# Optimization experiments

Hardware: AMD Instinct MI355X
Metric: run time of the kernel (lower is better)

Reference implementation:

```python
import jax, jax.numpy as jnp
import numpy as np

B, N, H, HS = 8, 96, 8, 32
NS = H * HS  # 256, also ES
EPS = 1e-5


def _linear(x, w, b):
    return x @ w + b  # w: [in, out]


def _ln(x, g, b):
    m = jnp.mean(x, axis=-1, keepdims=True)
    v = jnp.var(x, axis=-1, keepdims=True)
    return (x - m) * jax.lax.rsqrt(v + EPS) * g + b


def _sep_n(x):  # [B,N,NS] -> [B,H,N,HS]
    b, n, _ = x.shape
    return x.reshape(b, n, H, HS).transpose(0, 2, 1, 3)


def _sep_e(x):  # [B,N,N,ES] -> [B,H,N,N,HS]
    b, n, _, _ = x.shape
    return x.reshape(b, n, n, H, HS).transpose(0, 3, 1, 2, 4)


def setup_inputs() -> dict:
    key = jax.random.key(0)
    ks = jax.random.split(key, 32)
    s = 1.0 / np.sqrt(NS)
    d = {
        "node_tensors": jax.random.normal(ks[0], (B, N, NS), jnp.float32),
        "edge_tensors": jax.random.normal(ks[1], (B, N, N, NS), jnp.float32),
    }
    names = ["Wn", "We", "Wn1", "Wn2", "Wee"]
    for i, nm in enumerate(names):
        d[nm + "_w"] = jax.random.uniform(ks[2 + 2 * i], (3, NS, NS), jnp.float32, -s, s)
        d[nm + "_b"] = jax.random.uniform(ks[3 + 2 * i], (3, NS), jnp.float32, -s, s)
    for i, nm in enumerate(["NL1", "NL2", "EL1", "EL2"]):
        d[nm + "_w"] = jax.random.uniform(ks[12 + 2 * i], (NS, NS), jnp.float32, -s, s)
        d[nm + "_b"] = jax.random.uniform(ks[13 + 2 * i], (NS,), jnp.float32, -s, s)
    d["NLN1_g"] = jnp.ones((NS,), jnp.float32)
    d["NLN1_b"] = jnp.zeros((NS,), jnp.float32)
    d["ELN1_g"] = jnp.ones((NS,), jnp.float32)
    d["ELN1_b"] = jnp.zeros((NS,), jnp.float32)
    return d


def _forward(node_tensors, edge_tensors, Wn_w, Wn_b, We_w, We_b, Wn1_w, Wn1_b,
             Wn2_w, Wn2_b, Wee_w, Wee_b, NL1_w, NL1_b, NL2_w, NL2_b,
             EL1_w, EL1_b, EL2_w, EL2_b, NLN1_g, NLN1_b, ELN1_g, ELN1_b):
    scale = 1.0 / jnp.sqrt(jnp.float32(HS))
    b = node_tensors.shape[0]

    # --- node attention ---
    eQ = _sep_e(_linear(edge_tensors, We_w[0], We_b[0]))
    eK = _sep_e(_linear(edge_tensors, We_w[1], We_b[1]))
    eV = _sep_e(_linear(edge_tensors, We_w[2], We_b[2]))
    nQ = _sep_n(_linear(node_tensors, Wn_w[0], Wn_b[0]))
    nK = _sep_n(_linear(node_tensors, Wn_w[1], Wn_b[1]))
    nV = _sep_n(_linear(node_tensors, Wn_w[2], Wn_b[2]))

    Q = eQ + nQ[:, :, :, None, :]          # [B,H,N,N,HS]
    K = eK + nK[:, :, None, :, :]
    scores = jnp.einsum('bhijc,bhijc->bhij', Q, K) * scale
    attn = jax.nn.softmax(scores, axis=-1)
    V = eV + nV[:, :, None, :, :]
    new_nodes = jnp.einsum('bhij,bhijc->bhic', attn, V)   # [B,H,N,HS]
    attw = new_nodes.transpose(0, 2, 1, 3).reshape(b, N, NS)

    res = _linear(jax.nn.relu(_linear(attw, NL1_w, NL1_b)), NL2_w, NL2_b)
    node_out = _ln(node_tensors + res, NLN1_g, NLN1_b)

    # --- edge update ---
    n1Q = _sep_n(_linear(node_out, Wn1_w[0], Wn1_b[0]))
    n1K = _sep_n(_linear(node_out, Wn1_w[1], Wn1_b[1]))
    n1V = _sep_n(_linear(node_out, Wn1_w[2], Wn1_b[2]))
    n2Q = _sep_n(_linear(node_out, Wn2_w[0], Wn2_b[0]))
    n2K = _sep_n(_linear(node_out, Wn2_w[1], Wn2_b[1]))
    n2V = _sep_n(_linear(node_out, Wn2_w[2], Wn2_b[2]))
    eQe = _sep_e(_linear(edge_tensors, Wee_w[0], Wee_b[0]))
    eKe = _sep_e(_linear(edge_tensors, Wee_w[1], Wee_b[1]))
    eVe = _sep_e(_linear(edge_tensors, Wee_w[2], Wee_b[2]))

    Qe = eQe + n1Q[:, :, :, None, :] + n2Q[:, :, None, :, :]
    Ke = eKe + n1K[:, :, :, None, :] + n2K[:, :, None, :, :]
    se = jnp.einsum('bhijc,bhijc->bhij', Qe, Ke) * scale
    attn_e = jax.nn.silu(se)                               # [B,H,N,N]
    Ve = eVe + n1V[:, :, :, None, :] + n2V[:, :, None, :, :]
    new_edges = attn_e[..., None] * Ve                     # [B,H,N,N,HS]
    attw_e = new_edges.transpose(0, 2, 3, 1, 4).reshape(b, N, N, NS)

    res_e = _linear(jax.nn.relu(_linear(attw_e, EL1_w, EL1_b)), EL2_w, EL2_b)
    edge_out = _ln(edge_tensors + res_e, ELN1_g, ELN1_b)
    return node_out, edge_out


def reference(node_tensors, edge_tensors, Wn_w, Wn_b, We_w, We_b, Wn1_w, Wn1_b,
              Wn2_w, Wn2_b, Wee_w, Wee_b, NL1_w, NL1_b, NL2_w, NL2_b,
              EL1_w, EL1_b, EL2_w, EL2_b, NLN1_g, NLN1_b, ELN1_g, ELN1_b):
    return _forward(node_tensors, edge_tensors, Wn_w, Wn_b, We_w, We_b,
                    Wn1_w, Wn1_b, Wn2_w, Wn2_b, Wee_w, Wee_b, NL1_w, NL1_b,
                    NL2_w, NL2_b, EL1_w, EL1_b, EL2_w, EL2_b,
                    NLN1_g, NLN1_b, ELN1_g, ELN1_b)
```

## Files before the change

### kernel.cpp

```cpp
#include <hip/hip_runtime.h>


#define DI __device__ __forceinline__

typedef float f32x4 __attribute__((ext_vector_type(4)));
typedef short bf16x8 __attribute__((ext_vector_type(8)));

DI unsigned short f2bf(float f) {
  union { float f; unsigned u; } v; v.f = f;
  return (unsigned short)((v.u + 0x7FFFu + ((v.u >> 16) & 1u)) >> 16);
}
DI float bf2f(unsigned short h) {
  union { unsigned u; float f; } v; v.u = ((unsigned)h) << 16;
  return v.f;
}

#define LDE 264
#define SCALE 0.17677669529663687f

#define MFMA(A, B, C) __builtin_amdgcn_mfma_f32_16x16x32_bf16((A), (B), (C), 0, 0, 0)

__global__ __launch_bounds__(256)
void prep_and_qkv(const float* __restrict__ We_w, const float* __restrict__ Wee_w,
                  const float* __restrict__ EL1_w, const float* __restrict__ EL2_w,
                  const float* __restrict__ NL1_w, const float* __restrict__ NL2_w,
                  const float* __restrict__ Wn1_w, const float* __restrict__ Wn2_w,
                  unsigned short* __restrict__ fb,
                  const float* __restrict__ node, const float* __restrict__ Ww,
                  const float* __restrict__ Wb, float* __restrict__ nQ,
                  float* __restrict__ nK, float* __restrict__ nV)
{
  __shared__ float Wl[32 * 256];
  const int t = threadIdx.x;
  if (blockIdx.x < 128) {
    const int blk = blockIdx.x, kt = blk & 7, ms = blk >> 3;
    const float* src; unsigned short* dst; int NT, ntbase;
    if (ms < 3)       { src = We_w  + ms * 65536;        dst = fb;          NT = 48; ntbase = ms * 16; }
    else if (ms < 6)  { src = Wee_w + (ms - 3) * 65536;  dst = fb + 196608; NT = 48; ntbase = (ms - 3) * 16; }
    else if (ms == 6) { src = EL1_w;                     dst = fb + 393216; NT = 16; ntbase = 0; }
    else if (ms == 7) { src = EL2_w;                     dst = fb + 458752; NT = 16; ntbase = 0; }
    else if (ms == 8) { src = NL1_w;                     dst = fb + 524288; NT = 16; ntbase = 0; }
    else if (ms == 9) { src = NL2_w;                     dst = fb + 589824; NT = 16; ntbase = 0; }
    else if (ms < 13) { src = Wn1_w + (ms - 10) * 65536; dst = fb + 655360; NT = 48; ntbase = (ms - 10) * 16; }
    else              { src = Wn2_w + (ms - 13) * 65536; dst = fb + 851968; NT = 48; ntbase = (ms - 13) * 16; }
    for (int u = t; u < 32 * 64; u += 256) {
      const int r = u >> 6, c4 = (u & 63) << 2;
      *(float4*)(Wl + r * 256 + c4) = *(const float4*)(src + (kt * 32 + r) * 256 + c4);
    }
    __syncthreads();
    for (int u = t; u < 16 * 64; u += 256) {
      const int ntl = u >> 6, l = u & 63;
      const int kb = (l >> 4) << 3, c = ntl * 16 + (l & 15);
      unsigned short tmp[8];
      #pragma unroll
      for (int i = 0; i < 8; ++i) tmp[i] = f2bf(Wl[(kb + i) * 256 + c]);
      const int nt = ntbase + ntl;
      *(uint4*)(dst + ((size_t)(kt * NT + nt) * 64 + l) * 8) = *(const uint4*)tmp;
    }
  } else {
    float (*x)[256] = (float(*)[256])Wl;
    const int r0 = (blockIdx.x - 128) * 4;
    #pragma unroll
    for (int rr = 0; rr < 4; ++rr) x[rr][t] = node[(r0 + rr) * 256 + t];
    __syncthreads();
    float a0[4], a1[4], a2[4];
    #pragma unroll
    for (int rr = 0; rr < 4; ++rr) { a0[rr] = Wb[t]; a1[rr] = Wb[256 + t]; a2[rr] = Wb[512 + t]; }
    for (int k = 0; k < 256; ++k) {
      const float w0 = Ww[k * 256 + t], w1 = Ww[65536 + k * 256 + t], w2 = Ww[131072 + k * 256 + t];
      #pragma unroll
      for (int rr = 0; rr < 4; ++rr) {
        const float xv = x[rr][k];
        a0[rr] += xv * w0; a1[rr] += xv * w1; a2[rr] += xv * w2;
      }
    }
    const int h = t >> 5, c = t & 31;
    #pragma unroll
    for (int rr = 0; rr < 4; ++rr) {
      const int row = r0 + rr, b = row / 96, j = row - b * 96;
      const int oi = ((b * 8 + h) * 96 + j) * 32 + c;
      nQ[oi] = a0[rr]; nK[oi] = a1[rr]; nV[oi] = a2[rr];
    }
  }
}

__global__ __launch_bounds__(512, 2)
void node_attn(const float* __restrict__ edge, const float* __restrict__ We_b,
               const unsigned short* __restrict__ WeF,
               const float* __restrict__ nQ, const float* __restrict__ nK,
               const float* __restrict__ nV, float* __restrict__ attw)
{
  __shared__ unsigned short Elds[96 * LDE];
  __shared__ float sc[768];
  __shared__ float nQp[256];
  __shared__ float bias[768];

  const int tid = threadIdx.x, lane = tid & 63, wid = tid >> 6;
  const int b = blockIdx.x & 7, i = blockIdx.x >> 3;
  const size_t bi = (size_t)(b * 96 + i);

  if (tid < 256) nQp[tid] = nQ[((b * 8 + (tid >> 5)) * 96 + i) * 32 + (tid & 31)];
  for (int u = tid; u < 768; u += 512) bias[u] = We_b[u];

  const float* Erow = edge + bi * 24576;
  for (int u = tid; u < 96 * 64; u += 512) {
    const int j = u >> 6, g = u & 63;
    const float4 v = *(const float4*)(Erow + j * 256 + g * 4);
    const unsigned lo = (unsigned)f2bf(v.x) | ((unsigned)f2bf(v.y) << 16);
    const unsigned hi = (unsigned)f2bf(v.z) | ((unsigned)f2bf(v.w) << 16);
    *(uint2*)(Elds + j * LDE + g * 4) = make_uint2(lo, hi);
  }
  __syncthreads();

  {
    const int h = wid;
    const unsigned short* wq0 = WeF + ((2 * h) * 64 + lane) * 8;
    const unsigned short* wq1 = WeF + ((2 * h + 1) * 64 + lane) * 8;
    const unsigned short* wk0 = WeF + ((16 + 2 * h) * 64 + lane) * 8;
    const unsigned short* wk1 = WeF + ((17 + 2 * h) * 64 + lane) * 8;
    const int c0 = h * 32 + (lane & 15), c1 = c0 + 16;
    const float qb0 = bias[c0] + nQp[c0], qb1 = bias[c1] + nQp[c1];
    const float kb0 = bias[256 + c0], kb1 = bias[256 + c1];
    for (int pass = 0; pass < 2; ++pass) {
      const f32x4 z = {0.f, 0.f, 0.f, 0.f};
      f32x4 aq0[3] = {z, z, z}, aq1[3] = {z, z, z}, ak0[3] = {z, z, z}, ak1[3] = {z, z, z};
      __builtin_amdgcn_s_setprio(1);
      for (int kt = 0; kt < 8; ++kt) {
        const bf16x8 b0 = *(const bf16x8*)(wq0 + kt * 24576);
        const bf16x8 b1 = *(const bf16x8*)(wq1 + kt * 24576);
        const bf16x8 b2 = *(const bf16x8*)(wk0 + kt * 24576);
        const bf16x8 b3 = *(const bf16x8*)(wk1 + kt * 24576);
        #pragma unroll
        for (int m = 0; m < 3; ++m) {
          const int mt = pass * 3 + m;
          const bf16x8 afr = *(const bf16x8*)(Elds + (mt * 16 + (lane & 15)) * LDE
                                              + ((lane >> 4) << 3) + kt * 32);
          aq0[m] = MFMA(afr, b0, aq0[m]);
          aq1[m] = MFMA(afr, b1, aq1[m]);
          ak0[m] = MFMA(afr, b2, ak0[m]);
          ak1[m] = MFMA(afr, b3, ak1[m]);
        }
      }
      __builtin_amdgcn_s_setprio(0);
      #pragma unroll
      for (int m = 0; m < 3; ++m) {
        const int mt = pass * 3 + m;
        float prod[4];
        #pragma unroll
        for (int r = 0; r < 4; ++r) {
          const int j = mt * 16 + ((lane >> 4) << 2) + r;
          const int g = ((b * 8 + h) * 96 + j) * 32;
          const float k0v = ak0[m][r] + kb0 + nK[g + (lane & 15)];
          const float k1v = ak1[m][r] + kb1 + nK[g + 16 + (lane & 15)];
          prod[r] = (aq0[m][r] + qb0) * k0v + (aq1[m][r] + qb1) * k1v;
        }
        #pragma unroll
        for (int mm = 1; mm < 16; mm <<= 1) {
          #pragma unroll
          for (int r = 0; r < 4; ++r) prod[r] += __shfl_xor(prod[r], mm, 64);
        }
        if ((lane & 15) == 0) {
          #pragma unroll
          for (int r = 0; r < 4; ++r)
            sc[h * 96 + mt * 16 + ((lane >> 4) << 2) + r] = prod[r];
        }
      }
    }
  }

  const f32x4 z = {0.f, 0.f, 0.f, 0.f};
  f32x4 accB[6][2] = {{z, z}, {z, z}, {z, z}, {z, z}, {z, z}, {z, z}};
  {
    const unsigned short* wb0 = WeF + ((32 + wid) * 64 + lane) * 8;
    const unsigned short* wb1 = WeF + ((40 + wid) * 64 + lane) * 8;
    __builtin_amdgcn_s_setprio(1);
    for (int kt = 0; kt < 8; ++kt) {
      const bf16x8 b0 = *(const bf16x8*)(wb0 + kt * 24576);
      const bf16x8 b1 = *(const bf16x8*)(wb1 + kt * 24576);
      #pragma unroll
      for (int mt = 0; mt < 6; ++mt) {
        const bf16x8 afr = *(const bf16x8*)(Elds + (mt * 16 + (lane & 15)) * LDE
                                            + ((lane >> 4) << 3) + kt * 32);
        accB[mt][0] = MFMA(afr, b0, accB[mt][0]);
        accB[mt][1] = MFMA(afr, b1, accB[mt][1]);
      }
    }
    __builtin_amdgcn_s_setprio(0);
  }
  __syncthreads();

  {
    const int h = wid;
    const float s0 = sc[h * 96 + lane] * SCALE;
    const float s1 = (lane < 32) ? sc[h * 96 + 64 + lane] * SCALE : -1e30f;
    float mx = fmaxf(s0, s1);
    #pragma unroll
    for (int m = 1; m < 64; m <<= 1) mx = fmaxf(mx, __shfl_xor(mx, m, 64));
    const float e0 = __expf(s0 - mx);
    const float e1 = (lane < 32) ? __expf(s1 - mx) : 0.f;
    float sm = e0 + e1;
    #pragma unroll
    for (int m = 1; m < 64; m <<= 1) sm += __shfl_xor(sm, m, 64);
    const float inv = 1.f / sm;
    sc[h * 96 + lane] = e0 * inv;
    if (lane < 32) sc[h * 96 + 64 + lane] = e1 * inv;
  }
  __syncthreads();

  {
    const int col0 = wid * 16 + (lane & 15), col1 = col0 + 128;
    const int h0 = col0 >> 5, cc0 = col0 & 31;
    const int h1 = col1 >> 5, cc1 = col1 & 31;
    const float base0 = bias[512 + col0], base1 = bias[512 + col1];
    float nn[2] = {0.f, 0.f};
    #pragma unroll
    for (int mt = 0; mt < 6; ++mt) {
      #pragma unroll
      for (int r = 0; r < 4; ++r) {
        const int j = mt * 16 + ((lane >> 4) << 2) + r;
        const float v0 = accB[mt][0][r] + base0 + nV[((b * 8 + h0) * 96 + j) * 32 + cc0];
        const float v1 = accB[mt][1][r] + base1 + nV[((b * 8 + h1) * 96 + j) * 32 + cc1];
        nn[0] += sc[h0 * 96 + j] * v0;
        nn[1] += sc[h1 * 96 + j] * v1;
      }
    }
    #pragma unroll
    for (int s = 0; s < 2; ++s) {
      nn[s] += __shfl_xor(nn[s], 16, 64);
      nn[s] += __shfl_xor(nn[s], 32, 64);
    }
    if (lane < 16) {
      attw[bi * 256 + wid * 16 + lane] = nn[0];
      attw[bi * 256 + (wid + 8) * 16 + lane] = nn[1];
    }
  }
}

__global__ __launch_bounds__(256)
void node_tail(const float* __restrict__ attw, const float* __restrict__ node,
               const unsigned short* __restrict__ NL1F, const float* __restrict__ B1,
               const unsigned short* __restrict__ NL2F, const float* __restrict__ B2,
               const float* __restrict__ g, const float* __restrict__ be,
               const unsigned short* __restrict__ Wn1F, const float* __restrict__ P1b,
               const unsigned short* __restrict__ Wn2F, const float* __restrict__ P2b,
               float* __restrict__ node_out,
               float* __restrict__ n1Q, float* __restrict__ n1K, float* __restrict__ n1V,
               float* __restrict__ n2Q, float* __restrict__ n2K, float* __restrict__ n2V)
{
  __shared__ unsigned short Xl[16 * LDE];
  __shared__ unsigned short Hl[16 * LDE];
  __shared__ float bb[1024];
  __shared__ float p1b[768], p2b[768];
  __shared__ float psum[4][16], psq[4][16];
  __shared__ float statm[16], statr[16];

  const int t = threadIdx.x, lane = t & 63, w = t >> 6;
  const int bt = blockIdx.x, r0 = bt * 16;
  const int b = bt / 6, nbase = (bt % 6) * 16;

  bb[t] = B1[t]; bb[256 + t] = B2[t]; bb[512 + t] = g[t]; bb[768 + t] = be[t];
  for (int u = t; u < 768; u += 256) { p1b[u] = P1b[u]; p2b[u] = P2b[u]; }

  for (int u = t; u < 16 * 64; u += 256) {
    const int j = u >> 6, gg = u & 63;
    const float4 v = *(const float4*)(attw + (size_t)(r0 + j) * 256 + gg * 4);
    const unsigned lo = (unsigned)f2bf(v.x) | ((unsigned)f2bf(v.y) << 16);
    const unsigned hi = (unsigned)f2bf(v.z) | ((unsigned)f2bf(v.w) << 16);
    *(uint2*)(Xl + j * LDE + gg * 4) = make_uint2(lo, hi);
  }
  __syncthreads();

  const f32x4 z = {0.f, 0.f, 0.f, 0.f};

  {
    f32x4 a1[4] = {z, z, z, z};
    for (int kt = 0; kt < 8; ++kt) {
      const bf16x8 afr = *(const bf16x8*)(Xl + (lane & 15) * LDE + ((lane >> 4) << 3) + kt * 32);
      #pragma unroll
      for (int p = 0; p < 4; ++p) {
        const bf16x8 bf = *(const bf16x8*)(NL1F + (((kt << 4) + (w * 4 + p)) * 64 + lane) * 8);
        a1[p] = MFMA(afr, bf, a1[p]);
      }
    }
    #pragma unroll
    for (int p = 0; p < 4; ++p) {
      const int col = (w * 4 + p) * 16 + (lane & 15);
      const float bv = bb[col];
      #pragma unroll
      for (int r = 0; r < 4; ++r) {
        const int j = ((lane >> 4) << 2) + r;
        Hl[j * LDE + col] = f2bf(fmaxf(a1[p][r] + bv, 0.f));
      }
    }
  }
  __syncthreads();

  float xv[4][4];
  {
    f32x4 a2[4] = {z, z, z, z};
    for (int kt = 0; kt < 8; ++kt) {
      const bf16x8 afr = *(const bf16x8*)(Hl + (lane & 15) * LDE + ((lane >> 4) << 3) + kt * 32);
      #pragma unroll
      for (int p = 0; p < 4; ++p) {
        const bf16x8 bf = *(const bf16x8*)(NL2F + (((kt << 4) + (w * 4 + p)) * 64 + lane) * 8);
        a2[p] = MFMA(afr, bf, a2[p]);
      }
    }
    #pragma unroll
    for (int p = 0; p < 4; ++p) {
      const int col = (w * 4 + p) * 16 + (lane & 15);
      const float bv = bb[256 + col];
      #pragma unroll
      for (int r = 0; r < 4; ++r) {
        const int j = ((lane >> 4) << 2) + r;
        xv[p][r] = a2[p][r] + bv + node[(size_t)(r0 + j) * 256 + col];
      }
    }
    #pragma unroll
    for (int r = 0; r < 4; ++r) {
      float s = 0.f, q = 0.f;
      #pragma unroll
      for (int p = 0; p < 4; ++p) { s += xv[p][r]; q += xv[p][r] * xv[p][r]; }
      #pragma unroll
      for (int m = 1; m < 16; m <<= 1) { s += __shfl_xor(s, m, 64); q += __shfl_xor(q, m, 64); }
      if ((lane & 15) == 0) {
        const int rl = ((lane >> 4) << 2) + r;
        psum[w][rl] = s; psq[w][rl] = q;
      }
    }
  }
  __syncthreads();
  if (t < 16) {
    const float s = psum[0][t] + psum[1][t] + psum[2][t] + psum[3][t];
    const float q = psq[0][t] + psq[1][t] + psq[2][t] + psq[3][t];
    const float mean = s * (1.f / 256.f);
    statm[t] = mean;
    statr[t] = rsqrtf(q * (1.f / 256.f) - mean * mean + 1e-5f);
  }
  __syncthreads();
  #pragma unroll
  for (int p = 0; p < 4; ++p) {
    const int col = (w * 4 + p) * 16 + (lane & 15);
    const float gv = bb[512 + col], bv = bb[768 + col];
    #pragma unroll
    for (int r = 0; r < 4; ++r) {
      const int j = ((lane >> 4) << 2) + r;
      const float o = (xv[p][r] - statm[j]) * statr[j] * gv + bv;
      node_out[(size_t)(r0 + j) * 256 + col] = o;
      Xl[j * LDE + col] = f2bf(o);
    }
  }
  __syncthreads();

  bf16x8 xfr[8];
  #pragma unroll
  for (int kt = 0; kt < 8; ++kt)
    xfr[kt] = *(const bf16x8*)(Xl + (lane & 15) * LDE + ((lane >> 4) << 3) + kt * 32);
  #pragma unroll
  for (int ps = 0; ps < 2; ++ps) {
    const unsigned short* WF = ps ? Wn2F : Wn1F;
    const float* pb = ps ? p2b : p1b;
    f32x4 ac[12] = {z, z, z, z, z, z, z, z, z, z, z, z};
    __builtin_amdgcn_s_setprio(1);
    for (int kt = 0; kt < 8; ++kt) {
      #pragma unroll
      for (int m = 0; m < 12; ++m) {
        const int nt = w * 12 + m;
        const bf16x8 bf = *(const bf16x8*)(WF + ((kt * 48 + nt) * 64 + lane) * 8);
        ac[m] = MFMA(xfr[kt], bf, ac[m]);
      }
    }
    __builtin_amdgcn_s_setprio(0);
    #pragma unroll
    for (int m = 0; m < 12; ++m) {
      const int nt = w * 12 + m;
      const int colg = nt * 16 + (lane & 15);
      const int q = colg >> 8, cn = colg & 255, h = cn >> 5, c = cn & 31;
      float* o = (q == 0) ? (ps ? n2Q : n1Q)
               : (q == 1) ? (ps ? n2K : n1K)
                          : (ps ? n2V : n1V);
      const float bv = pb[colg];
      #pragma unroll
      for (int r = 0; r < 4; ++r) {
        const int j = ((lane >> 4) << 2) + r;
        o[((b * 8 + h) * 96 + nbase + j) * 32 + c] = ac[m][r] + bv;
      }
    }
  }
}

__global__ __launch_bounds__(512, 2)
void edge_update(const float* __restrict__ edge, const float* __restrict__ Wee_b,
                 const unsigned short* __restrict__ WeeF,
                 const unsigned short* __restrict__ EL1F,
                 const unsigned short* __restrict__ EL2F,
                 const float* __restrict__ EL1_b, const float* __restrict__ EL2_b,
                 const float* __restrict__ n1Q, const float* __restrict__ n1K, const float* __restrict__ n1V,
                 const float* __restrict__ n2Q, const float* __restrict__ n2K, const float* __restrict__ n2V,
                 const float* __restrict__ lng, const float* __restrict__ lnb,
                 float* __restrict__ edge_out)
{
  __shared__ unsigned short Elds[96 * LDE];
  __shared__ float se[768];
  __shared__ float bn1[768];
  __shared__ float b12[512];
  __shared__ float lg[256], lb[256];

  const int tid = threadIdx.x, lane = tid & 63, wid = tid >> 6;
  const int b = blockIdx.x & 7, i = blockIdx.x >> 3;
  const size_t bi = (size_t)(b * 96 + i);

  for (int u = tid; u < 768; u += 512) {
    const int q = u >> 8, cn = u & 255, h = cn >> 5, c = cn & 31;
    const float* s = (q == 0) ? n1Q : (q == 1) ? n1K : n1V;
    bn1[u] = Wee_b[u] + s[((b * 8 + h) * 96 + i) * 32 + c];
  }
  b12[tid] = (tid < 256) ? EL1_b[tid] : EL2_b[tid - 256];
  if (tid < 256) { lg[tid] = lng[tid]; lb[tid] = lnb[tid]; }

  const float* Erow = edge + bi * 24576;
  for (int u = tid; u < 96 * 64; u += 512) {
    const int j = u >> 6, g = u & 63;
    const float4 v = *(const float4*)(Erow + j * 256 + g * 4);
    const unsigned lo = (unsigned)f2bf(v.x) | ((unsigned)f2bf(v.y) << 16);
    const unsigned hi = (unsigned)f2bf(v.z) | ((unsigned)f2bf(v.w) << 16);
    *(uint2*)(Elds + j * LDE + g * 4) = make_uint2(lo, hi);
  }
  __syncthreads();

  {
    const int h = wid;
    const unsigned short* wq0 = WeeF + ((2 * h) * 64 + lane) * 8;
    const unsigned short* wq1 = WeeF + ((2 * h + 1) * 64 + lane) * 8;
    const unsigned short* wk0 = WeeF + ((16 + 2 * h) * 64 + lane) * 8;
    const unsigned short* wk1 = WeeF + ((17 + 2 * h) * 64 + lane) * 8;
    const int c0 = h * 32 + (lane & 15), c1 = c0 + 16;
    const float qb0 = bn1[c0], qb1 = bn1[c1];
    const float kb0 = bn1[256 + c0], kb1 = bn1[256 + c1];
    for (int pass = 0; pass < 2; ++pass) {
      const f32x4 z = {0.f, 0.f, 0.f, 0.f};
      f32x4 aq0[3] = {z, z, z}, aq1[3] = {z, z, z}, ak0[3] = {z, z, z}, ak1[3] = {z, z, z};
      __builtin_amdgcn_s_setprio(1);
      for (int kt = 0; kt < 8; ++kt) {
        const bf16x8 b0 = *(const bf16x8*)(wq0 + kt * 24576);
        const bf16x8 b1 = *(const bf16x8*)(wq1 + kt * 24576);
        const bf16x8 b2 = *(const bf16x8*)(wk0 + kt * 24576);
        const bf16x8 b3 = *(const bf16x8*)(wk1 + kt * 24576);
        #pragma unroll
        for (int m = 0; m < 3; ++m) {
          const int mt = pass * 3 + m;
          const bf16x8 afr = *(const bf16x8*)(Elds + (mt * 16 + (lane & 15)) * LDE
                                              + ((lane >> 4) << 3) + kt * 32);
          aq0[m] = MFMA(afr, b0, aq0[m]);
          aq1[m] = MFMA(afr, b1, aq1[m]);
          ak0[m] = MFMA(afr, b2, ak0[m]);
          ak1[m] = MFMA(afr, b3, ak1[m]);
        }
      }
      __builtin_amdgcn_s_setprio(0);
      #pragma unroll
      for (int m = 0; m < 3; ++m) {
        const int mt = pass * 3 + m;
        float prod[4];
        #pragma unroll
        for (int r = 0; r < 4; ++r) {
          const int j = mt * 16 + ((lane >> 4) << 2) + r;
          const int g = ((b * 8 + h) * 96 + j) * 32;
          const float q0v = aq0[m][r] + qb0 + n2Q[g + (lane & 15)];
          const float q1v = aq1[m][r] + qb1 + n2Q[g + 16 + (lane & 15)];
          const float k0v = ak0[m][r] + kb0 + n2K[g + (lane & 15)];
          const float k1v = ak1[m][r] + kb1 + n2K[g + 16 + (lane & 15)];
          prod[r] = q0v * k0v + q1v * k1v;
        }
        #pragma unroll
        for (int mm = 1; mm < 16; mm <<= 1) {
          #pragma unroll
          for (int r = 0; r < 4; ++r) prod[r] += __shfl_xor(prod[r], mm, 64);
        }
        if ((lane & 15) == 0) {
          #pragma unroll
          for (int r = 0; r < 4; ++r) {
            const float d = prod[r] * SCALE;
            se[h * 96 + mt * 16 + ((lane >> 4) << 2) + r] = d / (1.f + __expf(-d));
          }
        }
      }
    }
  }

  const f32x4 z = {0.f, 0.f, 0.f, 0.f};
  f32x4 acc[6][2] = {{z, z}, {z, z}, {z, z}, {z, z}, {z, z}, {z, z}};
  {
    const unsigned short* wb0 = WeeF + ((32 + wid) * 64 + lane) * 8;
    const unsigned short* wb1 = WeeF + ((40 + wid) * 64 + lane) * 8;
    __builtin_amdgcn_s_setprio(1);
    for (int kt = 0; kt < 8; ++kt) {
      const bf16x8 b0 = *(const bf16x8*)(wb0 + kt * 24576);
      const bf16x8 b1 = *(const bf16x8*)(wb1 + kt * 24576);
      #pragma unroll
      for (int mt = 0; mt < 6; ++mt) {
        const bf16x8 afr = *(const bf16x8*)(Elds + (mt * 16 + (lane & 15)) * LDE
                                            + ((lane >> 4) << 3) + kt * 32);
        acc[mt][0] = MFMA(afr, b0, acc[mt][0]);
        acc[mt][1] = MFMA(afr, b1, acc[mt][1]);
      }
    }
    __builtin_amdgcn_s_setprio(0);
  }
  __syncthreads();

  {
    const int col0 = wid * 16 + (lane & 15), col1 = col0 + 128;
    const int h0 = col0 >> 5, cc0 = col0 & 31;
    const int h1 = col1 >> 5, cc1 = col1 & 31;
    const float base0 = bn1[512 + col0], base1 = bn1[512 + col1];
    #pragma unroll
    for (int mt = 0; mt < 6; ++mt) {
      #pragma unroll
      for (int r = 0; r < 4; ++r) {
        const int j = mt * 16 + ((lane >> 4) << 2) + r;
        const float v0 = acc[mt][0][r] + base0 + n2V[((b * 8 + h0) * 96 + j) * 32 + cc0];
        const float v1 = acc[mt][1][r] + base1 + n2V[((b * 8 + h1) * 96 + j) * 32 + cc1];
        Elds[j * LDE + col0] = f2bf(se[h0 * 96 + j] * v0);
        Elds[j * LDE + col1] = f2bf(se[h1 * 96 + j] * v1);
      }
    }
  }
  __syncthreads();

  {
    #pragma unroll
    for (int mt = 0; mt < 6; ++mt) { acc[mt][0] = z; acc[mt][1] = z; }
    const unsigned short* wb0 = EL1F + (wid * 64 + lane) * 8;
    const unsigned short* wb1 = EL1F + ((wid + 8) * 64 + lane) * 8;
    __builtin_amdgcn_s_setprio(1);
    for (int kt = 0; kt < 8; ++kt) {
      const bf16x8 b0 = *(const bf16x8*)(wb0 + kt * 8192);
      const bf16x8 b1 = *(const bf16x8*)(wb1 + kt * 8192);
      #pragma unroll
      for (int mt = 0; mt < 6; ++mt) {
        const bf16x8 afr = *(const bf16x8*)(Elds + (mt * 16 + (lane & 15)) * LDE
                                            + ((lane >> 4) << 3) + kt * 32);
        acc[mt][0] = MFMA(afr, b0, acc[mt][0]);
        acc[mt][1] = MFMA(afr, b1, acc[mt][1]);
      }
    }
    __builtin_amdgcn_s_setprio(0);
    __syncthreads();
    const int col0 = wid * 16 + (lane & 15), col1 = col0 + 128;
    const float bv0 = b12[col0], bv1 = b12[col1];
    #pragma unroll
    for (int mt = 0; mt < 6; ++mt) {
      #pragma unroll
      for (int r = 0; r < 4; ++r) {
        const int j = mt * 16 + ((lane >> 4) << 2) + r;
        Elds[j * LDE + col0] = f2bf(fmaxf(acc[mt][0][r] + bv0, 0.f));
        Elds[j * LDE + col1] = f2bf(fmaxf(acc[mt][1][r] + bv1, 0.f));
      }
    }
  }
  __syncthreads();

  {
    #pragma unroll
    for (int mt = 0; mt < 6; ++mt) { acc[mt][0] = z; acc[mt][1] = z; }
    const unsigned short* wb0 = EL2F + (wid * 64 + lane) * 8;
    const unsigned short* wb1 = EL2F + ((wid + 8) * 64 + lane) * 8;
    __builtin_amdgcn_s_setprio(1);
    for (int kt = 0; kt < 8; ++kt) {
      const bf16x8 b0 = *(const bf16x8*)(wb0 + kt * 8192);
      const bf16x8 b1 = *(const bf16x8*)(wb1 + kt * 8192);
      #pragma unroll
      for (int mt = 0; mt < 6; ++mt) {
        const bf16x8 afr = *(const bf16x8*)(Elds + (mt * 16 + (lane & 15)) * LDE
                                            + ((lane >> 4) << 3) + kt * 32);
        acc[mt][0] = MFMA(afr, b0, acc[mt][0]);
        acc[mt][1] = MFMA(afr, b1, acc[mt][1]);
      }
    }
    __builtin_amdgcn_s_setprio(0);
    const int col0 = wid * 16 + (lane & 15), col1 = col0 + 128;
    const float bv0 = b12[256 + col0], bv1 = b12[256 + col1];
    const float g0 = lg[col0], g1 = lg[col1], be0 = lb[col0], be1 = lb[col1];
    __syncthreads();
    #pragma unroll
    for (int mt = 0; mt < 6; ++mt) {
      #pragma unroll
      for (int r = 0; r < 4; ++r) {
        const int j = mt * 16 + ((lane >> 4) << 2) + r;
        acc[mt][0][r] += bv0 + Erow[j * 256 + col0];
        acc[mt][1][r] += bv1 + Erow[j * 256 + col1];
      }
    }
    #pragma unroll
    for (int mt = 0; mt < 6; ++mt) {
      #pragma unroll
      for (int r = 0; r < 4; ++r) {
        float s = acc[mt][0][r] + acc[mt][1][r];
        float q = acc[mt][0][r] * acc[mt][0][r] + acc[mt][1][r] * acc[mt][1][r];
        #pragma unroll
        for (int m = 1; m < 16; m <<= 1) { s += __shfl_xor(s, m, 64); q += __shfl_xor(q, m, 64); }
        if ((lane & 15) == 0) {
          const int j = mt * 16 + ((lane >> 4) << 2) + r;
          se[wid * 96 + j] = s; bn1[wid * 96 + j] = q;
        }
      }
    }
    __syncthreads();
    if (tid < 96) {
      float s = 0.f, q = 0.f;
      #pragma unroll
      for (int w = 0; w < 8; ++w) { s += se[w * 96 + tid]; q += bn1[w * 96 + tid]; }
      const float mean = s * (1.f / 256.f);
      b12[tid] = mean;
      b12[96 + tid] = rsqrtf(q * (1.f / 256.f) - mean * mean + 1e-5f);
    }
    __syncthreads();
    #pragma unroll
    for (int mt = 0; mt < 6; ++mt) {
      #pragma unroll
      for (int r = 0; r < 4; ++r) {
        const int j = mt * 16 + ((lane >> 4) << 2) + r;
        const float mean = b12[j], rs = b12[96 + j];
        Elds[j * LDE + col0] = f2bf((acc[mt][0][r] - mean) * rs * g0 + be0);
        Elds[j * LDE + col1] = f2bf((acc[mt][1][r] - mean) * rs * g1 + be1);
      }
    }
  }
  __syncthreads();

  float* orow = edge_out + bi * 24576;
  for (int j = wid; j < 96; j += 8) {
    const uint2 pk = *(const uint2*)(Elds + j * LDE + (lane << 2));
    float4 o;
    o.x = bf2f((unsigned short)(pk.x & 0xffff));
    o.y = bf2f((unsigned short)(pk.x >> 16));
    o.z = bf2f((unsigned short)(pk.y & 0xffff));
    o.w = bf2f((unsigned short)(pk.y >> 16));
    *(float4*)(orow + j * 256 + (lane << 2)) = o;
  }
}

extern "C" void kernel_launch(void* const* d_in, const int* in_sizes, int n_in,
                              void* d_out, int out_size, void* d_ws, size_t ws_size,
                              hipStream_t stream)
{
  (void)in_sizes; (void)n_in; (void)out_size; (void)ws_size;

  const float* node   = (const float*)d_in[0];
  const float* edge   = (const float*)d_in[1];
  const float* Wn_w   = (const float*)d_in[2];
  const float* Wn_b   = (const float*)d_in[3];
  const float* We_w   = (const float*)d_in[4];
  const float* We_b   = (const float*)d_in[5];
  const float* Wn1_w  = (const float*)d_in[6];
  const float* Wn1_b  = (const float*)d_in[7];
  const float* Wn2_w  = (const float*)d_in[8];
  const float* Wn2_b  = (const float*)d_in[9];
  const float* Wee_w  = (const float*)d_in[10];
  const float* Wee_b  = (const float*)d_in[11];
  const float* NL1_w  = (const float*)d_in[12];
  const float* NL1_b  = (const float*)d_in[13];
  const float* NL2_w  = (const float*)d_in[14];
  const float* NL2_b  = (const float*)d_in[15];
  const float* EL1_w  = (const float*)d_in[16];
  const float* EL1_b  = (const float*)d_in[17];
  const float* EL2_w  = (const float*)d_in[18];
  const float* EL2_b  = (const float*)d_in[19];
  const float* NLN1_g = (const float*)d_in[20];
  const float* NLN1_b = (const float*)d_in[21];
  const float* ELN1_g = (const float*)d_in[22];
  const float* ELN1_b = (const float*)d_in[23];

  float* out = (float*)d_out;
  float* node_out = out;
  float* edge_out = out + 196608;

  float* wsf = (float*)d_ws;
  float* nQ  = wsf;                float* nK  = wsf + 196608;   float* nV  = wsf + 393216;
  float* n1Q = wsf + 589824;       float* n1K = wsf + 786432;   float* n1V = wsf + 983040;
  float* n2Q = wsf + 1179648;      float* n2K = wsf + 1376256;  float* n2V = wsf + 1572864;
  float* attw = wsf + 1769472;
  unsigned short* fb   = (unsigned short*)(wsf + 1966080);
  unsigned short* WeF  = fb;
  unsigned short* WeeF = fb + 196608;
  unsigned short* EL1F = fb + 393216;
  unsigned short* EL2F = fb + 458752;
  unsigned short* NL1F = fb + 524288;
  unsigned short* NL2F = fb + 589824;
  unsigned short* Wn1F = fb + 655360;
  unsigned short* Wn2F = fb + 851968;

  prep_and_qkv<<<320, 256, 0, stream>>>(We_w, Wee_w, EL1_w, EL2_w,
                                        NL1_w, NL2_w, Wn1_w, Wn2_w, fb,
                                        node, Wn_w, Wn_b, nQ, nK, nV);
  node_attn<<<768, 512, 0, stream>>>(edge, We_b, WeF, nQ, nK, nV, attw);
  node_tail<<<48, 256, 0, stream>>>(attw, node, NL1F, NL1_b, NL2F, NL2_b,
                                    NLN1_g, NLN1_b, Wn1F, Wn1_b, Wn2F, Wn2_b,
                                    node_out, n1Q, n1K, n1V, n2Q, n2K, n2V);
  edge_update<<<768, 512, 0, stream>>>(edge, Wee_b, WeeF, EL1F, EL2F,
                                       EL1_b, EL2_b, n1Q, n1K, n1V,
                                       n2Q, n2K, n2V, ELN1_g, ELN1_b, edge_out);
}
```

Measured before the change: 261.4 us.

## Split node QKV into MFMA kernel, shrink edge_update LDS for higher occupancy

```diff
diff --git a/kernel.cpp b/kernel.cpp
--- a/kernel.cpp
+++ b/kernel.cpp
@@ -21,65 +21,87 @@
 #define MFMA(A, B, C) __builtin_amdgcn_mfma_f32_16x16x32_bf16((A), (B), (C), 0, 0, 0)
 
 __global__ __launch_bounds__(256)
-void prep_and_qkv(const float* __restrict__ We_w, const float* __restrict__ Wee_w,
-                  const float* __restrict__ EL1_w, const float* __restrict__ EL2_w,
-                  const float* __restrict__ NL1_w, const float* __restrict__ NL2_w,
-                  const float* __restrict__ Wn1_w, const float* __restrict__ Wn2_w,
-                  unsigned short* __restrict__ fb,
-                  const float* __restrict__ node, const float* __restrict__ Ww,
-                  const float* __restrict__ Wb, float* __restrict__ nQ,
-                  float* __restrict__ nK, float* __restrict__ nV)
+void prep_frags(const float* __restrict__ We_w, const float* __restrict__ Wee_w,
+                const float* __restrict__ EL1_w, const float* __restrict__ EL2_w,
+                const float* __restrict__ NL1_w, const float* __restrict__ NL2_w,
+                const float* __restrict__ Wn1_w, const float* __restrict__ Wn2_w,
+                const float* __restrict__ Wn_w,
+                unsigned short* __restrict__ fb)
 {
   __shared__ float Wl[32 * 256];
   const int t = threadIdx.x;
-  if (blockIdx.x < 128) {
-    const int blk = blockIdx.x, kt = blk & 7, ms = blk >> 3;
-    const float* src; unsigned short* dst; int NT, ntbase;
-    if (ms < 3)       { src = We_w  + ms * 65536;        dst = fb;          NT = 48; ntbase = ms * 16; }
-    else if (ms < 6)  { src = Wee_w + (ms - 3) * 65536;  dst = fb + 196608; NT = 48; ntbase = (ms - 3) * 16; }
-    else if (ms == 6) { src = EL1_w;                     dst = fb + 393216; NT = 16; ntbase = 0; }
-    else if (ms == 7) { src = EL2_w;                     dst = fb + 458752; NT = 16; ntbase = 0; }
-    else if (ms == 8) { src = NL1_w;                     dst = fb + 524288; NT = 16; ntbase = 0; }
-    else if (ms == 9) { src = NL2_w;                     dst = fb + 589824; NT = 16; ntbase = 0; }
-    else if (ms < 13) { src = Wn1_w + (ms - 10) * 65536; dst = fb + 655360; NT = 48; ntbase = (ms - 10) * 16; }
-    else              { src = Wn2_w + (ms - 13) * 65536; dst = fb + 851968; NT = 48; ntbase = (ms - 13) * 16; }
-    for (int u = t; u < 32 * 64; u += 256) {
-      const int r = u >> 6, c4 = (u & 63) << 2;
-      *(float4*)(Wl + r * 256 + c4) = *(const float4*)(src + (kt * 32 + r) * 256 + c4);
-    }
-    __syncthreads();
-    for (int u = t; u < 16 * 64; u += 256) {
-      const int ntl = u >> 6, l = u & 63;
-      const int kb = (l >> 4) << 3, c = ntl * 16 + (l & 15);
-      unsigned short tmp[8];
-      #pragma unroll
-      for (int i = 0; i < 8; ++i) tmp[i] = f2bf(Wl[(kb + i) * 256 + c]);
-      const int nt = ntbase + ntl;
-      *(uint4*)(dst + ((size_t)(kt * NT + nt) * 64 + l) * 8) = *(const uint4*)tmp;
-    }
-  } else {
-    float (*x)[256] = (float(*)[256])Wl;
-    const int r0 = (blockIdx.x - 128) * 4;
-    #pragma unroll
-    for (int rr = 0; rr < 4; ++rr) x[rr][t] = node[(r0 + rr) * 256 + t];
-    __syncthreads();
-    float a0[4], a1[4], a2[4];
-    #pragma unroll
-    for (int rr = 0; rr < 4; ++rr) { a0[rr] = Wb[t]; a1[rr] = Wb[256 + t]; a2[rr] = Wb[512 + t]; }
-    for (int k = 0; k < 256; ++k) {
-      const float w0 = Ww[k * 256 + t], w1 = Ww[65536 + k * 256 + t], w2 = Ww[131072 + k * 256 + t];
-      #pragma unroll
-      for (int rr = 0; rr < 4; ++rr) {
-        const float xv = x[rr][k];
-        a0[rr] += xv * w0; a1[rr] += xv * w1; a2[rr] += xv * w2;
-      }
-    }
-    const int h = t >> 5, c = t & 31;
-    #pragma unroll
-    for (int rr = 0; rr < 4; ++rr) {
-      const int row = r0 + rr, b = row / 96, j = row - b * 96;
-      const int oi = ((b * 8 + h) * 96 + j) * 32 + c;
-      nQ[oi] = a0[rr]; nK[oi] = a1[rr]; nV[oi] = a2[rr];
+  const int blk = blockIdx.x, kt = blk & 7, ms = blk >> 3;
+  const float* src; unsigned short* dst; int NT, ntbase;
+  if (ms < 3)       { src = We_w  + ms * 65536;        dst = fb;           NT = 48; ntbase = ms * 16; }
+  else if (ms < 6)  { src = Wee_w + (ms - 3) * 65536;  dst = fb + 196608;  NT = 48; ntbase = (ms - 3) * 16; }
+  else if (ms == 6) { src = EL1_w;                     dst = fb + 393216;  NT = 16; ntbase = 0; }
+  else if (ms == 7) { src = EL2_w;                     dst = fb + 458752;  NT = 16; ntbase = 0; }
+  else if (ms == 8) { src = NL1_w;                     dst = fb + 524288;  NT = 16; ntbase = 0; }
+  else if (ms == 9) { src = NL2_w;                     dst = fb + 589824;  NT = 16; ntbase = 0; }
+  else if (ms < 13) { src = Wn1_w + (ms - 10) * 65536; dst = fb + 655360;  NT = 48; ntbase = (ms - 10) * 16; }
+  else if (ms < 16) { src = Wn2_w + (ms - 13) * 65536; dst = fb + 851968;  NT = 48; ntbase = (ms - 13) * 16; }
+  else              { src = Wn_w  + (ms - 16) * 65536; dst = fb + 1048576; NT = 48; ntbase = (ms - 16) * 16; }
+  for (int u = t; u < 32 * 64; u += 256) {
+    const int r = u >> 6, c4 = (u & 63) << 2;
+    *(float4*)(Wl + r * 256 + c4) = *(const float4*)(src + (kt * 32 + r) * 256 + c4);
+  }
+  __syncthreads();
+  for (int u = t; u < 16 * 64; u += 256) {
+    const int ntl = u >> 6, l = u & 63;
+    const int kb = (l >> 4) << 3, c = ntl * 16 + (l & 15);
+    unsigned short tmp[8];
+    #pragma unroll
+    for (int i = 0; i < 8; ++i) tmp[i] = f2bf(Wl[(kb + i) * 256 + c]);
+    const int nt = ntbase + ntl;
+    *(uint4*)(dst + ((size_t)(kt * NT + nt) * 64 + l) * 8) = *(const uint4*)tmp;
+  }
+}
+
+__global__ __launch_bounds__(256)
+void node_qkv(const float* __restrict__ node, const unsigned short* __restrict__ WnF,
+              const float* __restrict__ Wb, float* __restrict__ nQ,
+              float* __restrict__ nK, float* __restrict__ nV)
+{
+  __shared__ unsigned short Xl[16 * LDE];
+  const int t = threadIdx.x, lane = t & 63, w = t >> 6;
+  const int rb = blockIdx.x, r0 = rb * 16;
+  const int b = rb / 6, nbase = (rb % 6) * 16;
+
+  for (int u = t; u < 16 * 64; u += 256) {
+    const int j = u >> 6, gg = u & 63;
+    const float4 v = *(const float4*)(node + (size_t)(r0 + j) * 256 + gg * 4);
+    const unsigned lo = (unsigned)f2bf(v.x) | ((unsigned)f2bf(v.y) << 16);
+    const unsigned hi = (unsigned)f2bf(v.z) | ((unsigned)f2bf(v.w) << 16);
+    *(uint2*)(Xl + j * LDE + gg * 4) = make_uint2(lo, hi);
+  }
+  __syncthreads();
+
+  const f32x4 z = {0.f, 0.f, 0.f, 0.f};
+  bf16x8 xfr[8];
+  #pragma unroll
+  for (int kt = 0; kt < 8; ++kt)
+    xfr[kt] = *(const bf16x8*)(Xl + (lane & 15) * LDE + ((lane >> 4) << 3) + kt * 32);
+  f32x4 ac[12] = {z, z, z, z, z, z, z, z, z, z, z, z};
+  __builtin_amdgcn_s_setprio(1);
+  for (int kt = 0; kt < 8; ++kt) {
+    #pragma unroll
+    for (int m = 0; m < 12; ++m) {
+      const int nt = w * 12 + m;
+      const bf16x8 bf = *(const bf16x8*)(WnF + ((kt * 48 + nt) * 64 + lane) * 8);
+      ac[m] = MFMA(xfr[kt], bf, ac[m]);
+    }
+  }
+  __builtin_amdgcn_s_setprio(0);
+  #pragma unroll
+  for (int m = 0; m < 12; ++m) {
+    const int colg = (w * 12 + m) * 16 + (lane & 15);
+    const int q = colg >> 8, cn = colg & 255, h = cn >> 5, c = cn & 31;
+    float* o = (q == 0) ? nQ : (q == 1) ? nK : nV;
+    const float bv = Wb[colg];
+    #pragma unroll
+    for (int r = 0; r < 4; ++r) {
+      const int j = ((lane >> 4) << 2) + r;
+      o[((b * 8 + h) * 96 + nbase + j) * 32 + c] = ac[m][r] + bv;
     }
   }
 }
@@ -250,16 +272,14 @@
   __shared__ unsigned short Xl[16 * LDE];
   __shared__ unsigned short Hl[16 * LDE];
   __shared__ float bb[1024];
-  __shared__ float p1b[768], p2b[768];
   __shared__ float psum[4][16], psq[4][16];
   __shared__ float statm[16], statr[16];
 
   const int t = threadIdx.x, lane = t & 63, w = t >> 6;
-  const int bt = blockIdx.x, r0 = bt * 16;
-  const int b = bt / 6, nbase = (bt % 6) * 16;
+  const int ps = blockIdx.x & 1, rb = blockIdx.x >> 1;
+  const int r0 = rb * 16, b = rb / 6, nbase = (rb % 6) * 16;
 
   bb[t] = B1[t]; bb[256 + t] = B2[t]; bb[512 + t] = g[t]; bb[768 + t] = be[t];
-  for (int u = t; u < 768; u += 256) { p1b[u] = P1b[u]; p2b[u] = P2b[u]; }
 
   for (int u = t; u < 16 * 64; u += 256) {
     const int j = u >> 6, gg = u & 63;
@@ -346,20 +366,19 @@
     for (int r = 0; r < 4; ++r) {
       const int j = ((lane >> 4) << 2) + r;
       const float o = (xv[p][r] - statm[j]) * statr[j] * gv + bv;
-      node_out[(size_t)(r0 + j) * 256 + col] = o;
+      if (ps == 0) node_out[(size_t)(r0 + j) * 256 + col] = o;
       Xl[j * LDE + col] = f2bf(o);
     }
   }
   __syncthreads();
 
-  bf16x8 xfr[8];
-  #pragma unroll
-  for (int kt = 0; kt < 8; ++kt)
-    xfr[kt] = *(const bf16x8*)(Xl + (lane & 15) * LDE + ((lane >> 4) << 3) + kt * 32);
-  #pragma unroll
-  for (int ps = 0; ps < 2; ++ps) {
+  {
     const unsigned short* WF = ps ? Wn2F : Wn1F;
-    const float* pb = ps ? p2b : p1b;
+    const float* pb = ps ? P2b : P1b;
+    bf16x8 xfr[8];
+    #pragma unroll
+    for (int kt = 0; kt < 8; ++kt)
+      xfr[kt] = *(const bf16x8*)(Xl + (lane & 15) * LDE + ((lane >> 4) << 3) + kt * 32);
     f32x4 ac[12] = {z, z, z, z, z, z, z, z, z, z, z, z};
     __builtin_amdgcn_s_setprio(1);
     for (int kt = 0; kt < 8; ++kt) {
@@ -373,8 +392,7 @@
     __builtin_amdgcn_s_setprio(0);
     #pragma unroll
     for (int m = 0; m < 12; ++m) {
-      const int nt = w * 12 + m;
-      const int colg = nt * 16 + (lane & 15);
+      const int colg = (w * 12 + m) * 16 + (lane & 15);
       const int q = colg >> 8, cn = colg & 255, h = cn >> 5, c = cn & 31;
       float* o = (q == 0) ? (ps ? n2Q : n1Q)
                : (q == 1) ? (ps ? n2K : n1K)
@@ -389,7 +407,7 @@
   }
 }
 
-__global__ __launch_bounds__(512, 2)
+__global__ __launch_bounds__(512, 6)
 void edge_update(const float* __restrict__ edge, const float* __restrict__ Wee_b,
                  const unsigned short* __restrict__ WeeF,
                  const unsigned short* __restrict__ EL1F,
@@ -400,23 +418,14 @@
                  const float* __restrict__ lng, const float* __restrict__ lnb,
                  float* __restrict__ edge_out)
 {
-  __shared__ unsigned short Elds[96 * LDE];
-  __shared__ float se[768];
-  __shared__ float bn1[768];
-  __shared__ float b12[512];
-  __shared__ float lg[256], lb[256];
+  __shared__ float EldsF[12672];
+  __shared__ float seBuf[384];
+  unsigned short* Elds = (unsigned short*)EldsF;
+  unsigned short* se16 = (unsigned short*)seBuf;
 
   const int tid = threadIdx.x, lane = tid & 63, wid = tid >> 6;
   const int b = blockIdx.x & 7, i = blockIdx.x >> 3;
   const size_t bi = (size_t)(b * 96 + i);
-
-  for (int u = tid; u < 768; u += 512) {
-    const int q = u >> 8, cn = u & 255, h = cn >> 5, c = cn & 31;
-    const float* s = (q == 0) ? n1Q : (q == 1) ? n1K : n1V;
-    bn1[u] = Wee_b[u] + s[((b * 8 + h) * 96 + i) * 32 + c];
-  }
-  b12[tid] = (tid < 256) ? EL1_b[tid] : EL2_b[tid - 256];
-  if (tid < 256) { lg[tid] = lng[tid]; lb[tid] = lnb[tid]; }
 
   const float* Erow = edge + bi * 24576;
   for (int u = tid; u < 96 * 64; u += 512) {
@@ -435,11 +444,14 @@
     const unsigned short* wk0 = WeeF + ((16 + 2 * h) * 64 + lane) * 8;
     const unsigned short* wk1 = WeeF + ((17 + 2 * h) * 64 + lane) * 8;
     const int c0 = h * 32 + (lane & 15), c1 = c0 + 16;
-    const float qb0 = bn1[c0], qb1 = bn1[c1];
-    const float kb0 = bn1[256 + c0], kb1 = bn1[256 + c1];
-    for (int pass = 0; pass < 2; ++pass) {
+    const int nbI = ((b * 8 + h) * 96 + i) * 32;
+    const float qb0 = Wee_b[c0] + n1Q[nbI + (lane & 15)];
+    const float qb1 = Wee_b[c1] + n1Q[nbI + 16 + (lane & 15)];
+    const float kb0 = Wee_b[256 + c0] + n1K[nbI + (lane & 15)];
+    const float kb1 = Wee_b[256 + c1] + n1K[nbI + 16 + (lane & 15)];
+    for (int pass = 0; pass < 3; ++pass) {
       const f32x4 z = {0.f, 0.f, 0.f, 0.f};
-      f32x4 aq0[3] = {z, z, z}, aq1[3] = {z, z, z}, ak0[3] = {z, z, z}, ak1[3] = {z, z, z};
+      f32x4 aq0[2] = {z, z}, aq1[2] = {z, z}, ak0[2] = {z, z}, ak1[2] = {z, z};
       __builtin_amdgcn_s_setprio(1);
       for (int kt = 0; kt < 8; ++kt) {
         const bf16x8 b0 = *(const bf16x8*)(wq0 + kt * 24576);
@@ -447,8 +459,8 @@
         const bf16x8 b2 = *(const bf16x8*)(wk0 + kt * 24576);
         const bf16x8 b3 = *(const bf16x8*)(wk1 + kt * 24576);
         #pragma unroll
-        for (int m = 0; m < 3; ++m) {
-          const int mt = pass * 3 + m;
+        for (int m = 0; m < 2; ++m) {
+          const int mt = pass * 2 + m;
           const bf16x8 afr = *(const bf16x8*)(Elds + (mt * 16 + (lane & 15)) * LDE
                                               + ((lane >> 4) << 3) + kt * 32);
           aq0[m] = MFMA(afr, b0, aq0[m]);
@@ -459,8 +471,8 @@
       }
       __builtin_amdgcn_s_setprio(0);
       #pragma unroll
-      for (int m = 0; m < 3; ++m) {
-        const int mt = pass * 3 + m;
+      for (int m = 0; m < 2; ++m) {
+        const int mt = pass * 2 + m;
         float prod[4];
         #pragma unroll
         for (int r = 0; r < 4; ++r) {
@@ -481,7 +493,7 @@
           #pragma unroll
           for (int r = 0; r < 4; ++r) {
             const float d = prod[r] * SCALE;
-            se[h * 96 + mt * 16 + ((lane >> 4) << 2) + r] = d / (1.f + __expf(-d));
+            se16[h * 96 + mt * 16 + ((lane >> 4) << 2) + r] = f2bf(d / (1.f + __expf(-d)));
           }
         }
       }
@@ -513,7 +525,8 @@
     const int col0 = wid * 16 + (lane & 15), col1 = col0 + 128;
     const int h0 = col0 >> 5, cc0 = col0 & 31;
     const int h1 = col1 >> 5, cc1 = col1 & 31;
-    const float base0 = bn1[512 + col0], base1 = bn1[512 + col1];
+    const float base0 = Wee_b[512 + col0] + n1V[((b * 8 + h0) * 96 + i) * 32 + cc0];
+    const float base1 = Wee_b[512 + col1] + n1V[((b * 8 + h1) * 96 + i) * 32 + cc1];
     #pragma unroll
     for (int mt = 0; mt < 6; ++mt) {
       #pragma unroll
@@ -521,8 +534,8 @@
         const int j = mt * 16 + ((lane >> 4) << 2) + r;
         const float v0 = acc[mt][0][r] + base0 + n2V[((b * 8 + h0) * 96 + j) * 32 + cc0];
         const float v1 = acc[mt][1][r] + base1 + n2V[((b * 8 + h1) * 96 + j) * 32 + cc1];
-        Elds[j * LDE + col0] = f2bf(se[h0 * 96 + j] * v0);
-        Elds[j * LDE + col1] = f2bf(se[h1 * 96 + j] * v1);
+        Elds[j * LDE + col0] = f2bf(bf2f(se16[h0 * 96 + j]) * v0);
+        Elds[j * LDE + col1] = f2bf(bf2f(se16[h1 * 96 + j]) * v1);
       }
     }
   }
@@ -546,9 +559,9 @@
       }
     }
     __builtin_amdgcn_s_setprio(0);
+    const int col0 = wid * 16 + (lane & 15), col1 = col0 + 128;
+    const float bv0 = EL1_b[col0], bv1 = EL1_b[col1];
     __syncthreads();
-    const int col0 = wid * 16 + (lane & 15), col1 = col0 + 128;
-    const float bv0 = b12[col0], bv1 = b12[col1];
     #pragma unroll
     for (int mt = 0; mt < 6; ++mt) {
       #pragma unroll
@@ -580,8 +593,8 @@
     }
     __builtin_amdgcn_s_setprio(0);
     const int col0 = wid * 16 + (lane & 15), col1 = col0 + 128;
-    const float bv0 = b12[256 + col0], bv1 = b12[256 + col1];
-    const float g0 = lg[col0], g1 = lg[col1], be0 = lb[col0], be1 = lb[col1];
+    const float bv0 = EL2_b[col0], bv1 = EL2_b[col1];
+    const float g0 = lng[col0], g1 = lng[col1], be0 = lnb[col0], be1 = lnb[col1];
     __syncthreads();
     #pragma unroll
     for (int mt = 0; mt < 6; ++mt) {
@@ -602,7 +615,7 @@
         for (int m = 1; m < 16; m <<= 1) { s += __shfl_xor(s, m, 64); q += __shfl_xor(q, m, 64); }
         if ((lane & 15) == 0) {
           const int j = mt * 16 + ((lane >> 4) << 2) + r;
-          se[wid * 96 + j] = s; bn1[wid * 96 + j] = q;
+          EldsF[wid * 96 + j] = s; EldsF[768 + wid * 96 + j] = q;
         }
       }
     }
@@ -610,10 +623,10 @@
     if (tid < 96) {
       float s = 0.f, q = 0.f;
       #pragma unroll
-      for (int w = 0; w < 8; ++w) { s += se[w * 96 + tid]; q += bn1[w * 96 + tid]; }
+      for (int w = 0; w < 8; ++w) { s += EldsF[w * 96 + tid]; q += EldsF[768 + w * 96 + tid]; }
       const float mean = s * (1.f / 256.f);
-      b12[tid] = mean;
-      b12[96 + tid] = rsqrtf(q * (1.f / 256.f) - mean * mean + 1e-5f);
+      seBuf[tid] = mean;
+      seBuf[96 + tid] = rsqrtf(q * (1.f / 256.f) - mean * mean + 1e-5f);
     }
     __syncthreads();
     #pragma unroll
@@ -621,7 +634,7 @@
       #pragma unroll
       for (int r = 0; r < 4; ++r) {
         const int j = mt * 16 + ((lane >> 4) << 2) + r;
-        const float mean = b12[j], rs = b12[96 + j];
+        const float mean = seBuf[j], rs = seBuf[96 + j];
         Elds[j * LDE + col0] = f2bf((acc[mt][0][r] - mean) * rs * g0 + be0);
         Elds[j * LDE + col1] = f2bf((acc[mt][1][r] - mean) * rs * g1 + be1);
       }
@@ -690,12 +703,13 @@
   unsigned short* NL2F = fb + 589824;
   unsigned short* Wn1F = fb + 655360;
   unsigned short* Wn2F = fb + 851968;
-
-  prep_and_qkv<<<320, 256, 0, stream>>>(We_w, Wee_w, EL1_w, EL2_w,
-                                        NL1_w, NL2_w, Wn1_w, Wn2_w, fb,
-                                        node, Wn_w, Wn_b, nQ, nK, nV);
+  unsigned short* WnF  = fb + 1048576;
+
+  prep_frags<<<152, 256, 0, stream>>>(We_w, Wee_w, EL1_w, EL2_w, NL1_w, NL2_w,
+                                      Wn1_w, Wn2_w, Wn_w, fb);
+  node_qkv<<<48, 256, 0, stream>>>(node, WnF, Wn_b, nQ, nK, nV);
   node_attn<<<768, 512, 0, stream>>>(edge, We_b, WeF, nQ, nK, nV, attw);
-  node_tail<<<48, 256, 0, stream>>>(attw, node, NL1F, NL1_b, NL2F, NL2_b,
+  node_tail<<<96, 256, 0, stream>>>(attw, node, NL1F, NL1_b, NL2F, NL2_b,
                                     NLN1_g, NLN1_b, Wn1F, Wn1_b, Wn2F, Wn2_b,
                                     node_out, n1Q, n1K, n1V, n2Q, n2K, n2V);
   edge_update<<<768, 512, 0, stream>>>(edge, Wee_b, WeeF, EL1F, EL2F,
```

Measured after the change: 419.4 us. 60.4% more time.
